# Kernel tuning notes

Hardware: AMD Instinct MI355X
Metric: run time of the kernel (lower is better)

The kernel has to match this reference:

```python
import jax, jax.numpy as jnp
import numpy as np

B, N, C, H = 32, 512, 1024, 16
HD = C // H  # head_dim = 64
SCALE = HD ** -0.5


def setup_inputs() -> dict:
    key = jax.random.key(0)
    k1, k2, k3, k4 = jax.random.split(key, 4)
    # xavier_uniform bounds
    qkv_bound = (6.0 / (C + 3 * C)) ** 0.5
    proj_bound = 1.414 * (6.0 / (C + C)) ** 0.5
    return {
        "x": jax.random.normal(k1, (B, N, C), dtype=jnp.float32),
        "mask": jax.random.uniform(k2, (B, N), dtype=jnp.float32),
        "W_qkv": jax.random.uniform(k3, (3 * C, C), dtype=jnp.float32, minval=-qkv_bound, maxval=qkv_bound),
        "W_proj": jax.random.uniform(k4, (C, C), dtype=jnp.float32, minval=-proj_bound, maxval=proj_bound),
        "b_proj": jnp.zeros((C,), dtype=jnp.float32),
    }


def reference(x, mask, W_qkv, W_proj, b_proj):
    # qkv projection (no bias): [B,N,3C] -> [3,B,H,N,HD]
    qkv = jnp.einsum("bnc,dc->bnd", x, W_qkv)
    qkv = qkv.reshape(B, N, 3, H, HD).transpose(2, 0, 3, 1, 4)
    q, k, v = qkv[0] * SCALE, qkv[1], qkv[2]
    # attention scores [B,H,N,N] with additive row/col mask bias
    attn = jnp.einsum("bhqd,bhkd->bhqk", q, k)
    attn = attn + mask[:, None, None, :] + mask[:, None, :, None]
    attn = jax.nn.softmax(attn, axis=-1)
    out = jnp.einsum("bhqk,bhkd->bhqd", attn, v)
    out = out.transpose(0, 2, 1, 3).reshape(B, N, C)
    return jnp.einsum("bnc,dc->bnd", out, W_proj) + b_proj
```

## Files before the change

### kernel.cpp

```cpp
#include <hip/hip_runtime.h>
#include <stdint.h>

typedef unsigned short u16;
typedef __bf16 bf16x8 __attribute__((ext_vector_type(8)));
typedef float  f32x4  __attribute__((ext_vector_type(4)));
typedef float  f32x16 __attribute__((ext_vector_type(16)));
typedef unsigned int u32x4 __attribute__((ext_vector_type(4)));

#define MFMA16(a,b,c) __builtin_amdgcn_mfma_f32_16x16x32_bf16((a),(b),(c),0,0,0)
#define MFMA32(a,b,c) __builtin_amdgcn_mfma_f32_32x32x16_bf16((a),(b),(c),0,0,0)

#if __has_builtin(__builtin_amdgcn_exp2f)
#define EXP2F(x) __builtin_amdgcn_exp2f(x)
#else
#define EXP2F(x) exp2f(x)
#endif

__device__ __forceinline__ u16 f2b(float f) {
  unsigned int u = __builtin_bit_cast(unsigned int, f);
  u += 0x7fffu + ((u >> 16) & 1u);
  return (u16)(u >> 16);
}

__device__ __forceinline__ void gll16(const u16* g, u16* l) {
  __builtin_amdgcn_global_load_lds((const __attribute__((address_space(1))) unsigned int*)g,
                                   (__attribute__((address_space(3))) unsigned int*)l,
                                   16, 0, 0);
}

__device__ __forceinline__ unsigned cvtpk(float lo, float hi) {
  unsigned r;
  asm("v_cvt_pk_bf16_f32 %0, %1, %2" : "=v"(r) : "v"(lo), "v"(hi));
  return r;
}
__device__ __forceinline__ void pl32swap(unsigned &x, unsigned &y) {
  asm volatile("v_permlane32_swap_b32 %0, %1" : "+v"(x), "+v"(y));
}

#define BARR() __builtin_amdgcn_s_barrier()
#define SCHED0() __builtin_amdgcn_sched_barrier(0)
#define LGKM(N) do { asm volatile("s_waitcnt lgkmcnt(" #N ")" ::: "memory"); __builtin_amdgcn_sched_barrier(0); } while (0)
#define VMC(N) do { asm volatile("s_waitcnt vmcnt(" #N ")" ::: "memory"); __builtin_amdgcn_sched_barrier(0); } while (0)
#define PRIO1() __builtin_amdgcn_s_setprio(1)
#define PRIO0() __builtin_amdgcn_s_setprio(0)

__global__ __launch_bounds__(256)
void cvt_all(const float* __restrict__ X, const float* __restrict__ Wq,
             const float* __restrict__ Wp, u16* __restrict__ Xb,
             u16* __restrict__ Wqb, u16* __restrict__ Wpb)
{
  size_t i = (size_t)blockIdx.x * 256 + threadIdx.x;
  const float* src; u16* dst; size_t off;
  if (i < 4194304)       { src = X;  dst = Xb;  off = i; }
  else if (i < 4980736)  { src = Wq; dst = Wqb; off = i - 4194304; }
  else                   { src = Wp; dst = Wpb; off = i - 4980736; }
  float4 v = ((const float4*)src)[off];
  uint2 p;
  p.x = f2b(v.x) | ((unsigned)f2b(v.y) << 16);
  p.y = f2b(v.z) | ((unsigned)f2b(v.w) << 16);
  ((uint2*)dst)[off] = p;
}

#define DS_A(CUR, AF, RBASE) do { \
  _Pragma("unroll") for (int mt = 0; mt < 4; mt++) \
  _Pragma("unroll") for (int ks = 0; ks < 2; ks++) \
    AF[mt][ks] = *(const bf16x8*)((const char*)Asmem[CUR] + (RBASE) + aoff[mt][ks]); \
} while (0)

#define DS_B2(CUR, N0) do { \
  _Pragma("unroll") for (int nt = 0; nt < 2; nt++) \
  _Pragma("unroll") for (int ks = 0; ks < 2; ks++) \
    bfr[(N0) + nt][ks] = *(const bf16x8*)((const char*)Bsmem[CUR] + boff[(N0) + nt][ks]); \
} while (0)

#define MQ(MB, NB, AF) do { \
  _Pragma("unroll") for (int mt = 0; mt < 4; mt++) \
  _Pragma("unroll") for (int nt = 0; nt < 2; nt++) \
  _Pragma("unroll") for (int ks = 0; ks < 2; ks++) \
    acc[(MB) + mt][(NB) + nt] = MFMA16(AF[mt][ks], bfr[(NB) + nt][ks], acc[(MB) + mt][(NB) + nt]); \
} while (0)

#define HALF_ITER(CUR, TA, TB, ENDW) do { \
  DS_A(CUR, afl, 0); DS_B2(CUR, 0); SCHED0(); \
  DS_B2(CUR, 2); SCHED0(); \
  DS_A(CUR, afh, 8192); SCHED0(); \
  STAGE_A(TA, 0); STAGE_A(TA, 1); \
  LGKM(12); PRIO1(); MQ(0, 0, afl); PRIO0(); \
  LGKM(8);  PRIO1(); MQ(0, 2, afl); PRIO0(); \
  BARR();   \
  STAGE_B(TB, 0); STAGE_B(TB, 1); \
  LGKM(0);  PRIO1(); MQ(4, 0, afh); MQ(4, 2, afh); PRIO0(); \
  ENDW; \
  BARR(); \
} while (0)

template <int EPI>
__global__ __launch_bounds__(512, 2)
void gemm8p(const u16* __restrict__ Ag, const u16* __restrict__ Wg,
            u16* __restrict__ qb, u16* __restrict__ kb, u16* __restrict__ vT,
            const float* __restrict__ bias, float* __restrict__ outf, int nbx)
{
  __shared__ u16 Asmem[2][16384];
  __shared__ u16 Bsmem[2][16384];

  const int nwg = gridDim.x;
  const int cpx = nwg >> 3;
  const int bid = blockIdx.x;
  const int wg  = (bid & 7) * cpx + (bid >> 3);
  const int bx = wg % nbx, by = wg / nbx;
  const int row0 = by * 256, col0 = bx * 256;

  const int t = threadIdx.x;
  const int lane = t & 63, w = t >> 6;
  const int quad = lane >> 4, l16 = lane & 15;
  const int wm = w >> 2, wn = w & 3;
  const int sx = l16 & 7;

  const int srow = lane >> 3;
  const int scol = ((lane & 7) ^ srow) * 8;
  const u16* pA0 = Ag + (size_t)(row0 + w * 16 + srow) * 1024 + scol;
  const u16* pB0 = Wg + (size_t)(col0 + w * 16 + srow) * 1024 + scol;

  int aoff[4][2], boff[4][2];
#pragma unroll
  for (int mt = 0; mt < 4; mt++)
#pragma unroll
    for (int ks = 0; ks < 2; ks++) {
      int r = wm * 128 + mt * 16 + l16;
      aoff[mt][ks] = r * 128 + (((ks * 4 + quad) ^ sx) * 16);
    }
#pragma unroll
  for (int nt = 0; nt < 4; nt++)
#pragma unroll
    for (int ks = 0; ks < 2; ks++) {
      int r = wn * 64 + nt * 16 + l16;
      boff[nt][ks] = r * 128 + (((ks * 4 + quad) ^ sx) * 16);
    }

  f32x4 acc[8][4];
#pragma unroll
  for (int i = 0; i < 8; i++)
#pragma unroll
    for (int j = 0; j < 4; j++) acc[i][j] = f32x4{0.f, 0.f, 0.f, 0.f};

  auto STAGE_A = [&](int tile, int half) {
    if (tile >= 16) return;
    const u16* g = pA0 + (size_t)half * 131072 + tile * 64;
    u16* l = &Asmem[tile & 1][(half * 128 + w * 16) * 64];
    gll16(g, l);
    gll16(g + 8192, l + 512);
  };
  auto STAGE_B = [&](int tile, int half) {
    if (tile >= 16) return;
    const u16* g = pB0 + (size_t)half * 131072 + tile * 64;
    u16* l = &Bsmem[tile & 1][(half * 128 + w * 16) * 64];
    gll16(g, l);
    gll16(g + 8192, l + 512);
  };

  bf16x8 afl[4][2], afh[4][2], bfr[4][2];

  STAGE_B(0, 0); STAGE_B(0, 1); STAGE_A(0, 0); STAGE_A(0, 1);
  SCHED0();
  STAGE_B(1, 0); STAGE_B(1, 1);
  VMC(4); BARR();

#pragma unroll 1
  for (int i = 0; i < 7; ++i) {
    int t1 = 2 * i + 1;
    HALF_ITER(0, t1, t1 + 1, VMC(4));
    HALF_ITER(1, t1 + 1, t1 + 2, VMC(4));
  }
  HALF_ITER(0, 15, 16, VMC(0));
  HALF_ITER(1, 16, 17, ((void)0));

  const int tok_base = row0 + wm * 128;
  if constexpr (EPI == 0) {
#pragma unroll
    for (int nt = 0; nt < 4; nt++) {
      int d = col0 + wn * 64 + nt * 16;
      int part = d >> 10;
      int hh = (d >> 6) & 15;
      int hd = (d & 63) + l16;
      if (part == 2) {
#pragma unroll
        for (int mt = 0; mt < 8; mt++) {
          int nb = tok_base + mt * 16 + quad * 4;
          int bb = nb >> 9, nn = nb & 511;
          uint2 pk;
          pk.x = f2b(acc[mt][nt][0]) | ((unsigned)f2b(acc[mt][nt][1]) << 16);
          pk.y = f2b(acc[mt][nt][2]) | ((unsigned)f2b(acc[mt][nt][3]) << 16);
          *(uint2*)(vT + (((size_t)(bb * 16 + hh)) * 64 + hd) * 512 + nn) = pk;
        }
      } else {
        u16* dst = (part == 0) ? qb : kb;
        float sc = (part == 0) ? 0.125f : 1.0f;
#pragma unroll
        for (int mt = 0; mt < 8; mt++)
#pragma unroll
          for (int r = 0; r < 4; r++) {
            int tok = tok_base + mt * 16 + quad * 4 + r;
            int bb = tok >> 9, nn = tok & 511;
            dst[(((size_t)(bb * 16 + hh)) * 512 + nn) * 64 + hd] = f2b(acc[mt][nt][r] * sc);
          }
      }
    }
  } else {
#pragma unroll
    for (int nt = 0; nt < 4; nt++) {
      int d = col0 + wn * 64 + nt * 16 + l16;
      float bv = bias[d];
#pragma unroll
      for (int mt = 0; mt < 8; mt++)
#pragma unroll
        for (int r = 0; r < 4; r++) {
          int tok = tok_base + mt * 16 + quad * 4 + r;
          outf[(size_t)tok * 1024 + d] = acc[mt][nt][r] + bv;
        }
    }
  }
}

__global__ __launch_bounds__(256, 2)
void attn_kernel(const u16* __restrict__ qb, const u16* __restrict__ kb,
                 const u16* __restrict__ vT, const float* __restrict__ mask,
                 u16* __restrict__ ao)
{
  __shared__ u16 Kbuf[2][64 * 64];
  __shared__ u16 Vbuf[2][64 * 64];
  __shared__ float mk2[512];
  __shared__ float Lbuf[256];

  const int bid = blockIdx.x;
  const int wid = (bid & 7) * 128 + (bid >> 3);
  const int qt = wid & 1, bh = wid >> 1;
  const int b = bh >> 4, hh = bh & 15;

  const int t = threadIdx.x;
  const int lane = t & 63, w = t >> 6;
  const int l31 = lane & 31, hi = lane >> 5;
  const int sw = l31 & 7;

  const u16* Qp = qb + (size_t)bh * 512 * 64;
  const u16* Kp = kb + (size_t)bh * 512 * 64;
  const u16* Vp = vT + (size_t)bh * 64 * 512;

  for (int i = t; i < 512; i += 256) mk2[i] = mask[b * 512 + i] * 1.44269504f;

  const int qbase = qt * 256 + w * 64;
  bf16x8 qf[2][4];
#pragma unroll
  for (int g = 0; g < 2; g++)
#pragma unroll
    for (int dc = 0; dc < 4; dc++)
      qf[g][dc] = *(const bf16x8*)(Qp + (size_t)(qbase + g * 32 + l31) * 64 + dc * 16 + hi * 8);

  const int sr = lane >> 3, sc = lane & 7;
  const int cg = sc ^ sr;
  const u16* gk[2]; const u16* gv[2];
#pragma unroll
  for (int j = 0; j < 2; j++) {
    int r = w * 16 + j * 8 + sr;
    gk[j] = Kp + (size_t)r * 64 + cg * 8;
    gv[j] = Vp + (size_t)r * 512 + cg * 8;
  }

  f32x16 oacc[2][2];
#pragma unroll
  for (int g = 0; g < 2; g++)
#pragma unroll
    for (int i = 0; i < 16; i++) { oacc[g][0][i] = 0.f; oacc[g][1][i] = 0.f; }
  float lsum[2] = {0.f, 0.f};

  auto STAGE = [&](int tt, int buf) {
#pragma unroll
    for (int j = 0; j < 2; j++) {
      gll16(gk[j] + (size_t)tt * 4096, &Kbuf[buf][(w * 16 + j * 8) * 64]);
      gll16(gv[j] + (size_t)tt * 64,   &Vbuf[buf][(w * 16 + j * 8) * 64]);
    }
  };

  STAGE(0, 0);
  __syncthreads();

  for (int tt = 0; tt < 8; tt++) {
    const int cur = tt & 1;
    if (tt < 7) STAGE(tt + 1, cur ^ 1);
    const u16* Kb = Kbuf[cur];
    const u16* Vb = Vbuf[cur];
#pragma unroll
    for (int c = 0; c < 2; c++) {
      f32x16 s[2];
#pragma unroll
      for (int g = 0; g < 2; g++)
#pragma unroll
        for (int i = 0; i < 16; i++) s[g][i] = 0.f;
#pragma unroll
      for (int dc = 0; dc < 4; dc++) {
        int row = c * 32 + l31;
        bf16x8 kf = *(const bf16x8*)((const char*)Kb + row * 128 + (((2 * dc + hi) ^ sw) * 16));
        s[0] = MFMA32(kf, qf[0][dc], s[0]);
        s[1] = MFMA32(kf, qf[1][dc], s[1]);
      }
      const int kb0 = tt * 64 + c * 32;
      f32x4 mkv[4];
#pragma unroll
      for (int gg = 0; gg < 4; gg++) mkv[gg] = *(const f32x4*)(mk2 + kb0 + gg * 8 + hi * 4);

      bf16x8 af[2][2];
#pragma unroll
      for (int g = 0; g < 2; g++) {
        float p[16];
#pragma unroll
        for (int r = 0; r < 16; r++)
          p[r] = EXP2F(fmaf(s[g][r], 1.44269504f, mkv[r >> 2][r & 3]));
        float ls = 0.f;
#pragma unroll
        for (int r = 0; r < 16; r++) ls += p[r];
        lsum[g] += ls;

        unsigned d0a = cvtpk(p[0],  p[1]),  d1a = cvtpk(p[2],  p[3]);
        unsigned d2a = cvtpk(p[4],  p[5]),  d3a = cvtpk(p[6],  p[7]);
        unsigned d0b = cvtpk(p[8],  p[9]),  d1b = cvtpk(p[10], p[11]);
        unsigned d2b = cvtpk(p[12], p[13]), d3b = cvtpk(p[14], p[15]);
        pl32swap(d0a, d2a);
        pl32swap(d1a, d3a);
        pl32swap(d0b, d2b);
        pl32swap(d1b, d3b);
        u32x4 w0; w0.x = d0a; w0.y = d1a; w0.z = d2a; w0.w = d3a;
        u32x4 w1; w1.x = d0b; w1.y = d1b; w1.z = d2b; w1.w = d3b;
        af[g][0] = __builtin_bit_cast(bf16x8, w0);
        af[g][1] = __builtin_bit_cast(bf16x8, w1);
      }

#pragma unroll
      for (int kc = 0; kc < 2; kc++)
#pragma unroll
        for (int dc = 0; dc < 2; dc++) {
          int row = dc * 32 + l31;
          bf16x8 vf = *(const bf16x8*)((const char*)Vb + row * 128 + (((4 * c + 2 * kc + hi) ^ sw) * 16));
          oacc[0][dc] = MFMA32(af[0][kc], vf, oacc[0][dc]);
          oacc[1][dc] = MFMA32(af[1][kc], vf, oacc[1][dc]);
        }
    }
    __syncthreads();
  }

#pragma unroll
  for (int g = 0; g < 2; g++) {
    lsum[g] += __shfl_xor(lsum[g], 32);
    if (lane < 32) Lbuf[w * 64 + g * 32 + l31] = 1.0f / lsum[g];
  }
  __syncthreads();
  f32x4 inv4[2][4];
#pragma unroll
  for (int g = 0; g < 2; g++)
#pragma unroll
    for (int gg = 0; gg < 4; gg++)
      inv4[g][gg] = *(const f32x4*)(Lbuf + w * 64 + g * 32 + gg * 8 + hi * 4);

#pragma unroll
  for (int g = 0; g < 2; g++)
#pragma unroll
    for (int dc = 0; dc < 2; dc++)
#pragma unroll
      for (int r = 0; r < 16; r++) {
        int qrow = (r & 3) + 8 * (r >> 2) + 4 * hi;
        int n = qbase + g * 32 + qrow;
        int col = hh * 64 + dc * 32 + l31;
        ao[((size_t)(b * 512 + n)) * 1024 + col] = f2b(oacc[g][dc][r] * inv4[g][r >> 2][r & 3]);
      }
}

extern "C" void kernel_launch(void* const* d_in, const int* in_sizes, int n_in,
                              void* d_out, int out_size, void* d_ws, size_t ws_size,
                              hipStream_t stream) {
  const float* x     = (const float*)d_in[0];
  const float* mask  = (const float*)d_in[1];
  const float* Wqkv  = (const float*)d_in[2];
  const float* Wproj = (const float*)d_in[3];
  const float* bproj = (const float*)d_in[4];
  float* out = (float*)d_out;

  u16* qb  = (u16*)d_ws;
  u16* kb  = qb + 16777216;
  u16* vT  = kb + 16777216;
  u16* XbAo = vT + 16777216;
  u16* Wqb = XbAo + 16777216;
  u16* Wpb = Wqb + 3145728;

  cvt_all<<<20480, 256, 0, stream>>>(x, Wqkv, Wproj, XbAo, Wqb, Wpb);
  gemm8p<0><<<768, 512, 0, stream>>>(XbAo, Wqb, qb, kb, vT, nullptr, nullptr, 12);
  attn_kernel<<<1024, 256, 0, stream>>>(qb, kb, vT, mask, XbAo);
  gemm8p<1><<<256, 512, 0, stream>>>(XbAo, Wpb, nullptr, nullptr, nullptr, bproj, out, 4);
}
```

Baseline: 326.4 us.

## Use dedicated 128x128-tile projection GEMM and batch four float4s per thread in conversion

The output projection now runs in a new 128x128-tile kernel with 1024 blocks of 256 threads, replacing the 256x256-tile template instance that launched only 256 workgroups. The goal is better CU occupancy and load balance on the final GEMM. The new kernel uses a simpler double-buffered loop with full waits each iteration, so it loses some of the overlap the old pipeline had. The conversion kernel also makes each thread handle four float4s instead of one, cutting the launch to a quarter of the blocks.

```diff
diff --git a/kernel.cpp b/kernel.cpp
--- a/kernel.cpp
+++ b/kernel.cpp
@@ -49,16 +49,22 @@
              const float* __restrict__ Wp, u16* __restrict__ Xb,
              u16* __restrict__ Wqb, u16* __restrict__ Wpb)
 {
-  size_t i = (size_t)blockIdx.x * 256 + threadIdx.x;
+  size_t base = (size_t)blockIdx.x * 1024;
   const float* src; u16* dst; size_t off;
-  if (i < 4194304)       { src = X;  dst = Xb;  off = i; }
-  else if (i < 4980736)  { src = Wq; dst = Wqb; off = i - 4194304; }
-  else                   { src = Wp; dst = Wpb; off = i - 4980736; }
-  float4 v = ((const float4*)src)[off];
-  uint2 p;
-  p.x = f2b(v.x) | ((unsigned)f2b(v.y) << 16);
-  p.y = f2b(v.z) | ((unsigned)f2b(v.w) << 16);
-  ((uint2*)dst)[off] = p;
+  if (base < 4194304)       { src = X;  dst = Xb;  off = base; }
+  else if (base < 4980736)  { src = Wq; dst = Wqb; off = base - 4194304; }
+  else                      { src = Wp; dst = Wpb; off = base - 4980736; }
+  off += threadIdx.x;
+  float4 v[4];
+#pragma unroll
+  for (int j = 0; j < 4; j++) v[j] = ((const float4*)src)[off + j * 256];
+#pragma unroll
+  for (int j = 0; j < 4; j++) {
+    uint2 p;
+    p.x = f2b(v[j].x) | ((unsigned)f2b(v[j].y) << 16);
+    p.y = f2b(v[j].z) | ((unsigned)f2b(v[j].w) << 16);
+    ((uint2*)dst)[off + j * 256] = p;
+  }
 }
 
 #define DS_A(CUR, AF, RBASE) do { \
@@ -94,11 +100,10 @@
   BARR(); \
 } while (0)
 
-template <int EPI>
 __global__ __launch_bounds__(512, 2)
 void gemm8p(const u16* __restrict__ Ag, const u16* __restrict__ Wg,
             u16* __restrict__ qb, u16* __restrict__ kb, u16* __restrict__ vT,
-            const float* __restrict__ bias, float* __restrict__ outf, int nbx)
+            int nbx)
 {
   __shared__ u16 Asmem[2][16384];
   __shared__ u16 Bsmem[2][16384];
@@ -175,49 +180,129 @@
   HALF_ITER(1, 16, 17, ((void)0));
 
   const int tok_base = row0 + wm * 128;
-  if constexpr (EPI == 0) {
-#pragma unroll
-    for (int nt = 0; nt < 4; nt++) {
-      int d = col0 + wn * 64 + nt * 16;
-      int part = d >> 10;
-      int hh = (d >> 6) & 15;
-      int hd = (d & 63) + l16;
-      if (part == 2) {
-#pragma unroll
-        for (int mt = 0; mt < 8; mt++) {
-          int nb = tok_base + mt * 16 + quad * 4;
-          int bb = nb >> 9, nn = nb & 511;
-          uint2 pk;
-          pk.x = f2b(acc[mt][nt][0]) | ((unsigned)f2b(acc[mt][nt][1]) << 16);
-          pk.y = f2b(acc[mt][nt][2]) | ((unsigned)f2b(acc[mt][nt][3]) << 16);
-          *(uint2*)(vT + (((size_t)(bb * 16 + hh)) * 64 + hd) * 512 + nn) = pk;
-        }
-      } else {
-        u16* dst = (part == 0) ? qb : kb;
-        float sc = (part == 0) ? 0.125f : 1.0f;
-#pragma unroll
-        for (int mt = 0; mt < 8; mt++)
-#pragma unroll
-          for (int r = 0; r < 4; r++) {
-            int tok = tok_base + mt * 16 + quad * 4 + r;
-            int bb = tok >> 9, nn = tok & 511;
-            dst[(((size_t)(bb * 16 + hh)) * 512 + nn) * 64 + hd] = f2b(acc[mt][nt][r] * sc);
-          }
+#pragma unroll
+  for (int nt = 0; nt < 4; nt++) {
+    int d = col0 + wn * 64 + nt * 16;
+    int part = d >> 10;
+    int hh = (d >> 6) & 15;
+    int hd = (d & 63) + l16;
+    if (part == 2) {
+#pragma unroll
+      for (int mt = 0; mt < 8; mt++) {
+        int nb = tok_base + mt * 16 + quad * 4;
+        int bb = nb >> 9, nn = nb & 511;
+        uint2 pk;
+        pk.x = f2b(acc[mt][nt][0]) | ((unsigned)f2b(acc[mt][nt][1]) << 16);
+        pk.y = f2b(acc[mt][nt][2]) | ((unsigned)f2b(acc[mt][nt][3]) << 16);
+        *(uint2*)(vT + (((size_t)(bb * 16 + hh)) * 64 + hd) * 512 + nn) = pk;
       }
-    }
-  } else {
-#pragma unroll
-    for (int nt = 0; nt < 4; nt++) {
-      int d = col0 + wn * 64 + nt * 16 + l16;
-      float bv = bias[d];
+    } else {
+      u16* dst = (part == 0) ? qb : kb;
+      float sc = (part == 0) ? 0.125f : 1.0f;
 #pragma unroll
       for (int mt = 0; mt < 8; mt++)
 #pragma unroll
         for (int r = 0; r < 4; r++) {
           int tok = tok_base + mt * 16 + quad * 4 + r;
-          outf[(size_t)tok * 1024 + d] = acc[mt][nt][r] + bv;
+          int bb = tok >> 9, nn = tok & 511;
+          dst[(((size_t)(bb * 16 + hh)) * 512 + nn) * 64 + hd] = f2b(acc[mt][nt][r] * sc);
         }
     }
+  }
+}
+
+__global__ __launch_bounds__(256)
+void proj128(const u16* __restrict__ Ag, const u16* __restrict__ Wg,
+             const float* __restrict__ bias, float* __restrict__ outf)
+{
+  __shared__ u16 Asmem[2][8192];
+  __shared__ u16 Bsmem[2][8192];
+
+  const int bid = blockIdx.x;
+  const int wg  = (bid & 7) * 128 + (bid >> 3);
+  const int bx = wg & 7, by = wg >> 3;
+  const int row0 = by * 128, col0 = bx * 128;
+
+  const int t = threadIdx.x;
+  const int lane = t & 63, w = t >> 6;
+  const int quad = lane >> 4, l16 = lane & 15;
+  const int wm = w >> 1, wn = w & 1;
+  const int sx = l16 & 7;
+
+  const int srow = lane >> 3;
+  const int scol = ((lane & 7) ^ srow) * 8;
+  const u16* pA0 = Ag + (size_t)(row0 + w * 32 + srow) * 1024 + scol;
+  const u16* pB0 = Wg + (size_t)(col0 + w * 32 + srow) * 1024 + scol;
+
+  int aoff[4][2], boff[4][2];
+#pragma unroll
+  for (int mt = 0; mt < 4; mt++)
+#pragma unroll
+    for (int ks = 0; ks < 2; ks++) {
+      int r = wm * 64 + mt * 16 + l16;
+      aoff[mt][ks] = r * 128 + (((ks * 4 + quad) ^ sx) * 16);
+    }
+#pragma unroll
+  for (int nt = 0; nt < 4; nt++)
+#pragma unroll
+    for (int ks = 0; ks < 2; ks++) {
+      int r = wn * 64 + nt * 16 + l16;
+      boff[nt][ks] = r * 128 + (((ks * 4 + quad) ^ sx) * 16);
+    }
+
+  f32x4 acc[4][4];
+#pragma unroll
+  for (int i = 0; i < 4; i++)
+#pragma unroll
+    for (int j = 0; j < 4; j++) acc[i][j] = f32x4{0.f, 0.f, 0.f, 0.f};
+
+  auto STAGE = [&](int tile) {
+    if (tile >= 16) return;
+    int buf = tile & 1;
+#pragma unroll
+    for (int j = 0; j < 4; j++) {
+      gll16(pA0 + (size_t)j * 8192 + tile * 64, &Asmem[buf][(w * 32 + j * 8) * 64]);
+      gll16(pB0 + (size_t)j * 8192 + tile * 64, &Bsmem[buf][(w * 32 + j * 8) * 64]);
+    }
+  };
+
+  bf16x8 af[4][2], bfr[4][2];
+
+  STAGE(0);
+  VMC(0); BARR();
+
+#pragma unroll 1
+  for (int T = 0; T < 16; ++T) {
+    const int cur = T & 1;
+    STAGE(T + 1);
+#pragma unroll
+    for (int mt = 0; mt < 4; mt++)
+#pragma unroll
+      for (int ks = 0; ks < 2; ks++)
+        af[mt][ks] = *(const bf16x8*)((const char*)Asmem[cur] + aoff[mt][ks]);
+#pragma unroll
+    for (int nt = 0; nt < 4; nt++)
+#pragma unroll
+      for (int ks = 0; ks < 2; ks++)
+        bfr[nt][ks] = *(const bf16x8*)((const char*)Bsmem[cur] + boff[nt][ks]);
+    LGKM(0);
+    PRIO1(); MQ(0, 0, af); MQ(0, 2, af); PRIO0();
+    VMC(0);
+    BARR();
+  }
+
+  const int tok_base = row0 + wm * 64;
+#pragma unroll
+  for (int nt = 0; nt < 4; nt++) {
+    int d = col0 + wn * 64 + nt * 16 + l16;
+    float bv = bias[d];
+#pragma unroll
+    for (int mt = 0; mt < 4; mt++)
+#pragma unroll
+      for (int r = 0; r < 4; r++) {
+        int tok = tok_base + mt * 16 + quad * 4 + r;
+        outf[(size_t)tok * 1024 + d] = acc[mt][nt][r] + bv;
+      }
   }
 }
 
@@ -389,8 +474,8 @@
   u16* Wqb = XbAo + 16777216;
   u16* Wpb = Wqb + 3145728;
 
-  cvt_all<<<20480, 256, 0, stream>>>(x, Wqkv, Wproj, XbAo, Wqb, Wpb);
-  gemm8p<0><<<768, 512, 0, stream>>>(XbAo, Wqb, qb, kb, vT, nullptr, nullptr, 12);
+  cvt_all<<<5120, 256, 0, stream>>>(x, Wqkv, Wproj, XbAo, Wqb, Wpb);
+  gemm8p<<<768, 512, 0, stream>>>(XbAo, Wqb, qb, kb, vT, 12);
   attn_kernel<<<1024, 256, 0, stream>>>(qb, kb, vT, mask, XbAo);
-  gemm8p<1><<<256, 512, 0, stream>>>(XbAo, Wpb, nullptr, nullptr, nullptr, bproj, out, 4);
-}
+  proj128<<<1024, 256, 0, stream>>>(XbAo, Wpb, bproj, out);
+}
```

Result: slower. 342.4 us (+4.9%).
